# Kernel optimization log

Hardware: AMD Instinct MI355X
Metric: run time of the kernel (lower is better)

The kernel has to match this reference:

```python
import jax, jax.numpy as jnp
import numpy as np

# --- config (Qwen3-Next linear attention defaults) ---
B, S, H = 1, 256, 2048
NK, NV, DK, DV, K = 4, 32, 128, 128, 4
KEY_DIM = NK * DK          # 512
VAL_DIM = NV * DV          # 4096
CONV_DIM = 2 * KEY_DIM + VAL_DIM  # 5120
EPS = 1e-6


def setup_inputs() -> dict:
    key = jax.random.key(0)
    ks = jax.random.split(key, 8)
    rn = lambda k, shape, sc: jax.random.normal(k, shape, jnp.float32) * sc
    return {
        "hidden_states": jax.random.normal(ks[0], (B, S, H), jnp.float32),
        "w_qkvz": rn(ks[1], (2 * KEY_DIM + 2 * VAL_DIM, H), 0.02),  # in_proj_qkvz weight
        "w_ba": rn(ks[2], (2 * NV, H), 0.02),                        # in_proj_ba weight
        "w_out": rn(ks[3], (H, VAL_DIM), 0.02),                      # out_proj weight
        "conv_w": rn(ks[4], (CONV_DIM, 1, K), 0.1),                  # depthwise conv weight [C,1,K]
        "dt_bias": jnp.ones((NV,), jnp.float32),
        "A_log": jnp.zeros((NV,), jnp.float32),
        "norm_w": jnp.ones((DV,), jnp.float32),
    }


def reference(hidden_states, w_qkvz, w_ba, w_out, conv_w, dt_bias, A_log, norm_w):
    b, s, _ = hidden_states.shape
    # input projections (Linear without bias: x @ W.T)
    qkvz = hidden_states @ w_qkvz.T                      # [B,S,9216]
    ba = hidden_states @ w_ba.T                          # [B,S,64]
    q, k, v, z = jnp.split(qkvz, [KEY_DIM, 2 * KEY_DIM, 2 * KEY_DIM + VAL_DIM], axis=-1)
    beta, alpha = jnp.split(ba, 2, axis=-1)              # each [B,S,NV]

    # causal depthwise conv over concat(q,k,v), then silu
    qkv = jnp.concatenate([q, k, v], axis=-1).transpose(0, 2, 1)   # [B,C,S]
    qkv = jax.lax.conv_general_dilated(
        qkv, conv_w, window_strides=(1,), padding=[(K - 1, 0)],
        dimension_numbers=("NCH", "OIH", "NCH"), feature_group_count=CONV_DIM)
    qkv = jax.nn.silu(qkv).transpose(0, 2, 1)            # [B,S,C]
    q, k, v = jnp.split(qkv, [KEY_DIM, 2 * KEY_DIM], axis=-1)

    q = q.reshape(b, s, NK, DK)
    k = k.reshape(b, s, NK, DK)
    v = v.reshape(b, s, NV, DV)
    z = z.reshape(b, s, NV, DV)

    # GQA-style head expansion (repeat_interleave)
    ratio = NV // NK
    q = jnp.repeat(q, ratio, axis=2)                     # [B,S,NV,DK]
    k = jnp.repeat(k, ratio, axis=2)

    # NOTE: original computes g = -softplus(-A_log - alpha) but never uses it (dead code).
    beta_g = jax.nn.sigmoid(beta + dt_bias)[..., None]   # [B,S,NV,1]
    q = q * (DK ** -0.5)

    # naive delta-rule: full outer-product tensor + cumsum (memory-bound)
    kv = jnp.einsum("bsnk,bsnv->bsnkv", k, v * beta_g)   # [B,S,NV,DK,DV]
    out = jnp.einsum("bsnk,bsnkv->bsnv", q, jnp.cumsum(kv, axis=1))  # [B,S,NV,DV]

    # gated RMSNorm over head_v_dim in fp32
    of = out.astype(jnp.float32)
    var = jnp.mean(of * of, axis=-1, keepdims=True)
    of = of * jax.lax.rsqrt(var + EPS) * norm_w
    of = of * jax.nn.silu(z.astype(jnp.float32))

    return of.reshape(b, s, VAL_DIM) @ w_out.T           # [B,S,H]
```

## Files before the change

kernel.cpp:

```cpp
#include <hip/hip_runtime.h>
#include <hip/hip_bf16.h>

#define S_LEN   256
#define HID     2048
#define NVH     32
#define DKD     128
#define DVD     128
#define KEYDIM  512
#define VALDIM  4096
#define CONVDIM 5120
#define QKVZ_N  9216
#define EPS_F   1e-6f

typedef __attribute__((ext_vector_type(8))) short bf16x8;
typedef __attribute__((ext_vector_type(4))) float f32x4;

__device__ __forceinline__ unsigned short f2bf(float f) {
    union { float f; unsigned int i; } v; v.f = f;
    unsigned int x = v.i;
    return (unsigned short)((x + 0x7FFFu + ((x >> 16) & 1u)) >> 16);
}
__device__ __forceinline__ unsigned int pk2(float x, float y) {
    union { __hip_bfloat162 h; unsigned int u; } c;
    c.h = __float22bfloat162_rn(float2{x, y});
    return c.u;
}
__device__ __forceinline__ bf16x8 pack_bf8(float4 lo, float4 hi) {
    union { uint4 u; bf16x8 h; } c;
    c.u.x = pk2(lo.x, lo.y); c.u.y = pk2(lo.z, lo.w);
    c.u.z = pk2(hi.x, hi.y); c.u.w = pk2(hi.z, hi.w);
    return c.h;
}
__device__ __forceinline__ void gl_lds16(const void* g, void* l) {
    __builtin_amdgcn_global_load_lds(
        (const __attribute__((address_space(1))) unsigned int*)g,
        (__attribute__((address_space(3))) unsigned int*)l,
        16, 0, 0);
}

template<int NT>
__global__ __launch_bounds__(256, 2)
void gemm_db(const unsigned short* __restrict__ A, const float* __restrict__ B,
             float* __restrict__ Cpart, int N, int K, int kc) {
    __shared__ __align__(16) unsigned short As[2][128][64];
    __shared__ __align__(16) float Bs[2][NT][64];

    const int tid  = threadIdx.x;
    const int lane = tid & 63, wave = tid >> 6;
    const int wm = wave >> 1, wn = wave & 1;
    const int quad = lane >> 4, l16 = lane & 15;
    const int m0 = blockIdx.y * 128, n0 = blockIdx.x * NT;
    const int kbeg = blockIdx.z * kc;
    const int niter = kc >> 6;

    const int a_ro = lane >> 3;
    const int a_gc = (lane & 7) ^ a_ro;
    const int b_ro = lane >> 4;
    const int b_cs = lane & 15;

    f32x4 acc[4][2];
#pragma unroll
    for (int i = 0; i < 4; i++)
#pragma unroll
        for (int j = 0; j < 2; j++) acc[i][j] = (f32x4){0.f, 0.f, 0.f, 0.f};

    auto stage = [&](int buf, int kk) {
#pragma unroll
        for (int t = 0; t < 4; ++t) {
            int rbase = wave * 32 + t * 8;
            gl_lds16(A + (size_t)(m0 + rbase + a_ro) * K + kk + a_gc * 8,
                     &As[buf][rbase][0]);
        }
#pragma unroll
        for (int t = 0; t < NT / 16; ++t) {
            int rbase = wave * (NT / 4) + t * 4;
            int r = rbase + b_ro;
            int gc = b_cs ^ (r & 7);
            gl_lds16(B + (size_t)(n0 + r) * K + kk + gc * 4,
                     &Bs[buf][rbase][0]);
        }
    };

    auto compute = [&](int buf) {
#pragma unroll
        for (int ks = 0; ks < 2; ++ks) {
            bf16x8 af[4];
#pragma unroll
            for (int i = 0; i < 4; ++i) {
                int r = wm * 64 + i * 16 + l16;
                int c = (ks * 4 + quad) ^ (l16 & 7);
                af[i] = *(const bf16x8*)(&As[buf][r][c * 8]);
            }
#pragma unroll
            for (int j = 0; j < 2; ++j) {
                int r = wn * 32 + j * 16 + l16;
                int x = l16 & 7;
                int c0 = (ks * 8 + quad * 2) ^ x;
                int c1 = (ks * 8 + quad * 2 + 1) ^ x;
                float4 lo = *(const float4*)(&Bs[buf][r][c0 * 4]);
                float4 hi = *(const float4*)(&Bs[buf][r][c1 * 4]);
                bf16x8 bfr = pack_bf8(lo, hi);
#pragma unroll
                for (int i = 0; i < 4; ++i)
                    acc[i][j] = __builtin_amdgcn_mfma_f32_16x16x32_bf16(af[i], bfr, acc[i][j], 0, 0, 0);
            }
        }
    };

    stage(0, kbeg);
    __syncthreads();
    for (int it = 0; it < niter; ++it) {
        if (it + 1 < niter) stage((it + 1) & 1, kbeg + (it + 1) * 64);
        compute(it & 1);
        __syncthreads();
    }

    float* C = Cpart + (size_t)blockIdx.z * 256 * N;
#pragma unroll
    for (int i = 0; i < 4; i++)
#pragma unroll
        for (int j = 0; j < 2; j++)
#pragma unroll
            for (int r = 0; r < 4; r++) {
                int row = m0 + wm * 64 + i * 16 + quad * 4 + r;
                int col = n0 + wn * 32 + j * 16 + l16;
                C[(size_t)row * N + col] = acc[i][j][r];
            }
}

template<int P>
__global__ void reduce_sum(const float* __restrict__ part, float* __restrict__ out, int n) {
    int i = (blockIdx.x * 256 + threadIdx.x) * 4;
    if (i >= n) return;
    float4 s = *(const float4*)(part + i);
#pragma unroll
    for (int p = 1; p < P; p++) {
        float4 v = *(const float4*)(part + (size_t)p * n + i);
        s.x += v.x; s.y += v.y; s.z += v.z; s.w += v.w;
    }
    *(float4*)(out + i) = s;
}

__global__ __launch_bounds__(256)
void ba_proj_cvt(const float* __restrict__ hs, const float* __restrict__ w_ba,
                 float* __restrict__ ba, unsigned short* __restrict__ abf) {
    int s = blockIdx.x;
    int n = threadIdx.x & 63, seg = threadIdx.x >> 6;
    const float* x = hs + (size_t)s * HID + seg * 512;
    const float* w = w_ba + (size_t)n * HID + seg * 512;
    float acc = 0.f;
#pragma unroll 4
    for (int k = 0; k < 512; k += 4) {
        float4 xv = *(const float4*)(x + k);
        float4 wv = *(const float4*)(w + k);
        acc += xv.x * wv.x + xv.y * wv.y + xv.z * wv.z + xv.w * wv.w;
    }
    __shared__ float parts[4][64];
    parts[seg][n] = acc;
    {
        int d = threadIdx.x * 8;
        const float4* p = (const float4*)(hs + (size_t)s * HID + d);
        float4 a = p[0], b = p[1];
        uint4 r;
        r.x = pk2(a.x, a.y); r.y = pk2(a.z, a.w);
        r.z = pk2(b.x, b.y); r.w = pk2(b.z, b.w);
        *(uint4*)(abf + (size_t)s * HID + d) = r;
    }
    __syncthreads();
    if (threadIdx.x < 64)
        ba[s * 64 + threadIdx.x] = parts[0][threadIdx.x] + parts[1][threadIdx.x]
                                 + parts[2][threadIdx.x] + parts[3][threadIdx.x];
}

template<int P>
__global__ __launch_bounds__(256)
void sum_conv(const float* __restrict__ part, const float* __restrict__ conv_w,
              float* __restrict__ conv, float* __restrict__ zs) {
    const int s0 = blockIdx.y * 16;
    const int c  = blockIdx.x * 1024 + threadIdx.x * 4;
    auto sum4 = [&](int s) {
        const float* p = part + (size_t)s * QKVZ_N + c;
        float4 v = *(const float4*)p;
#pragma unroll
        for (int q = 1; q < P; q++) {
            float4 w = *(const float4*)(p + (size_t)q * S_LEN * QKVZ_N);
            v.x += w.x; v.y += w.y; v.z += w.z; v.w += w.w;
        }
        return v;
    };
    if (c < CONVDIM) {
        float4 cw[4];
#pragma unroll
        for (int i = 0; i < 4; ++i) cw[i] = *(const float4*)(conv_w + (size_t)(c + i) * 4);
        float4 w0{0,0,0,0}, w1{0,0,0,0}, w2{0,0,0,0};
        for (int s = (s0 >= 3 ? s0 - 3 : 0); s < s0; ++s) { w0 = w1; w1 = w2; w2 = sum4(s); }
        for (int s = s0; s < s0 + 16; ++s) {
            float4 w3 = sum4(s);
            float4 o;
            o.x = w0.x * cw[0].x + w1.x * cw[0].y + w2.x * cw[0].z + w3.x * cw[0].w;
            o.y = w0.y * cw[1].x + w1.y * cw[1].y + w2.y * cw[1].z + w3.y * cw[1].w;
            o.z = w0.z * cw[2].x + w1.z * cw[2].y + w2.z * cw[2].z + w3.z * cw[2].w;
            o.w = w0.w * cw[3].x + w1.w * cw[3].y + w2.w * cw[3].z + w3.w * cw[3].w;
            o.x = o.x / (1.f + __expf(-o.x));
            o.y = o.y / (1.f + __expf(-o.y));
            o.z = o.z / (1.f + __expf(-o.z));
            o.w = o.w / (1.f + __expf(-o.w));
            *(float4*)(conv + (size_t)s * CONVDIM + c) = o;
            w0 = w1; w1 = w2; w2 = w3;
        }
    } else {
        for (int s = s0; s < s0 + 16; ++s) {
            float4 v = sum4(s);
            *(float4*)(zs + (size_t)s * VALDIM + (c - CONVDIM)) = v;
        }
    }
}

__global__ __launch_bounds__(256)
void scores_k(const float* __restrict__ conv, const float* __restrict__ ba,
              const float* __restrict__ dt_bias, float* __restrict__ scores) {
    if (blockIdx.x > blockIdx.y) return;
    int hk = blockIdx.z;
    int s0 = blockIdx.y * 16, t0 = blockIdx.x * 16;
    __shared__ float Qs[16][132], Ks[16][132];
    int tid = threadIdx.x;
    int qoff = hk * DKD;
    int koff = KEYDIM + hk * DKD;
    for (int idx = tid; idx < 16 * 128; idx += 256) {
        int i = idx >> 7, d = idx & 127;
        Qs[i][d] = conv[(size_t)(s0 + i) * CONVDIM + qoff + d];
        Ks[i][d] = conv[(size_t)(t0 + i) * CONVDIM + koff + d];
    }
    __syncthreads();
    int tx = tid & 15, ty = tid >> 4;
    int s = s0 + ty, t = t0 + tx;
    float dot = 0.f;
    for (int d = 0; d < 128; d++) dot += Qs[ty][d] * Ks[tx][d];
    float base = (t <= s) ? dot * 0.08838834764831845f : 0.f;
#pragma unroll
    for (int v = 0; v < 8; v++) {
        int n = hk * 8 + v;
        float b = ba[t * 64 + n] + dt_bias[n];
        float bg = 1.f / (1.f + __expf(-b));
        scores[((size_t)n * 256 + s) * 256 + t] = base * bg;
    }
}

__global__ __launch_bounds__(256)
void attn_rms(const float* __restrict__ scores, const float* __restrict__ conv,
              const float* __restrict__ zs, const float* __restrict__ norm_w,
              unsigned short* __restrict__ normed) {
    int n = blockIdx.y, s0 = blockIdx.x * 16;
    int voff = 2 * KEYDIM + n * DVD;
    __shared__ float Ss[16][17];
    __shared__ float Vs[16][132];
    int tid = threadIdx.x, sy = tid >> 4, dx = tid & 15;
    float acc[8] = {0.f, 0.f, 0.f, 0.f, 0.f, 0.f, 0.f, 0.f};
    for (int t0 = 0; t0 <= s0; t0 += 16) {
        Ss[sy][dx] = scores[((size_t)n * 256 + s0 + sy) * 256 + t0 + dx];
        const float* vp = conv + (size_t)(t0 + sy) * CONVDIM + voff + dx * 8;
        *(float4*)&Vs[sy][dx * 8]     = *(const float4*)vp;
        *(float4*)&Vs[sy][dx * 8 + 4] = *(const float4*)(vp + 4);
        __syncthreads();
#pragma unroll
        for (int j = 0; j < 16; j++) {
            float sv = Ss[sy][j];
#pragma unroll
            for (int r = 0; r < 8; r++) acc[r] += sv * Vs[j][dx + 16 * r];
        }
        __syncthreads();
    }
    float ssq = 0.f;
#pragma unroll
    for (int r = 0; r < 8; r++) ssq += acc[r] * acc[r];
#pragma unroll
    for (int m = 1; m <= 8; m <<= 1) ssq += __shfl_xor(ssq, m, 64);
    float inv = rsqrtf(ssq * (1.f / 128.f) + EPS_F);
    int s = s0 + sy;
#pragma unroll
    for (int r = 0; r < 8; r++) {
        int d = dx + 16 * r;
        float z = zs[(size_t)s * VALDIM + n * DVD + d];
        float sz = z / (1.f + __expf(-z));
        float v = acc[r] * inv * norm_w[d] * sz;
        normed[((size_t)s * NVH + n) * DVD + d] = f2bf(v);
    }
}

extern "C" void kernel_launch(void* const* d_in, const int* in_sizes, int n_in,
                              void* d_out, int out_size, void* d_ws, size_t ws_size,
                              hipStream_t stream) {
    const float* hs      = (const float*)d_in[0];
    const float* w_qkvz  = (const float*)d_in[1];
    const float* w_ba    = (const float*)d_in[2];
    const float* w_out   = (const float*)d_in[3];
    const float* conv_w  = (const float*)d_in[4];
    const float* dt_bias = (const float*)d_in[5];
    const float* norm_w  = (const float*)d_in[7];

    char* ws = (char*)d_ws;
    unsigned short* abf = (unsigned short*)ws; ws += (size_t)S_LEN * HID * 2;
    float* ba   = (float*)ws;  ws += (size_t)S_LEN * 64 * 4;
    float* conv = (float*)ws;  ws += (size_t)S_LEN * CONVDIM * 4;
    float* zs   = (float*)ws;  ws += (size_t)S_LEN * VALDIM * 4;
    char* regB = ws;
    const bool big = ws_size >= (size_t)50 * 1024 * 1024;
    const int sk1 = big ? 4 : 2;
    const int sk2 = big ? 8 : 4;
    float* scratch1 = (float*)regB;
    unsigned short* normed = (unsigned short*)regB;
    float* scratch2 = (float*)(regB + 2097152);
    float* scores   = (float*)(regB + 2097152 + (size_t)sk2 * 2097152);

    ba_proj_cvt<<<S_LEN, 256, 0, stream>>>(hs, w_ba, ba, abf);
    gemm_db<64><<<dim3(QKVZ_N / 64, 2, sk1), 256, 0, stream>>>(abf, w_qkvz, scratch1, QKVZ_N, HID, HID / sk1);
    if (big) sum_conv<4><<<dim3(9, 16), 256, 0, stream>>>(scratch1, conv_w, conv, zs);
    else     sum_conv<2><<<dim3(9, 16), 256, 0, stream>>>(scratch1, conv_w, conv, zs);
    scores_k<<<dim3(16, 16, 4), 256, 0, stream>>>(conv, ba, dt_bias, scores);
    attn_rms<<<dim3(16, NVH), 256, 0, stream>>>(scores, conv, zs, norm_w, normed);
    gemm_db<64><<<dim3(HID / 64, 2, sk2), 256, 0, stream>>>(normed, w_out, scratch2, HID, VALDIM, VALDIM / sk2);
    if (big) reduce_sum<8><<<(S_LEN * HID) / 1024, 256, 0, stream>>>(scratch2, (float*)d_out, S_LEN * HID);
    else     reduce_sum<4><<<(S_LEN * HID) / 1024, 256, 0, stream>>>(scratch2, (float*)d_out, S_LEN * HID);
}
```

Baseline: 244.7 us.

## Use full-M single-buffer GEMM tiles, deeper split-K, and triangular score grid

The GEMM kernel now covers all 256 rows per block with a single LDS buffer instead of two 128-row double-buffered tiles. Each B tile is then loaded once per block rather than twice, the LDS footprint per block shrinks, and three blocks per CU are requested. The output projection switches to 32-wide N tiles with twice the split-K factor, and sum_conv uses smaller sequence chunks. scores_k now launches only the lower-triangular tile pairs instead of launching the full grid and exiting early. The risks are losing load/compute overlap without double buffering, more partial-sum traffic in the reduction, and a larger workspace requirement for the big path.

Measured after the change: 253.8 us. 1.04x slower.

```diff
diff --git a/kernel.cpp b/kernel.cpp
--- a/kernel.cpp
+++ b/kernel.cpp
@@ -39,37 +39,37 @@
 }
 
 template<int NT>
-__global__ __launch_bounds__(256, 2)
-void gemm_db(const unsigned short* __restrict__ A, const float* __restrict__ B,
+__global__ __launch_bounds__(256, 3)
+void gemm_sn(const unsigned short* __restrict__ A, const float* __restrict__ B,
              float* __restrict__ Cpart, int N, int K, int kc) {
-    __shared__ __align__(16) unsigned short As[2][128][64];
-    __shared__ __align__(16) float Bs[2][NT][64];
+    __shared__ __align__(16) unsigned short As[256][64];
+    __shared__ __align__(16) float Bs[NT][64];
 
     const int tid  = threadIdx.x;
     const int lane = tid & 63, wave = tid >> 6;
-    const int wm = wave >> 1, wn = wave & 1;
     const int quad = lane >> 4, l16 = lane & 15;
-    const int m0 = blockIdx.y * 128, n0 = blockIdx.x * NT;
-    const int kbeg = blockIdx.z * kc;
+    const int n0 = blockIdx.x * NT;
+    const int kbeg = blockIdx.y * kc;
     const int niter = kc >> 6;
+    constexpr int NB = NT / 16;
 
     const int a_ro = lane >> 3;
     const int a_gc = (lane & 7) ^ a_ro;
     const int b_ro = lane >> 4;
     const int b_cs = lane & 15;
 
-    f32x4 acc[4][2];
+    f32x4 acc[4][NB];
 #pragma unroll
     for (int i = 0; i < 4; i++)
 #pragma unroll
-        for (int j = 0; j < 2; j++) acc[i][j] = (f32x4){0.f, 0.f, 0.f, 0.f};
-
-    auto stage = [&](int buf, int kk) {
-#pragma unroll
-        for (int t = 0; t < 4; ++t) {
-            int rbase = wave * 32 + t * 8;
-            gl_lds16(A + (size_t)(m0 + rbase + a_ro) * K + kk + a_gc * 8,
-                     &As[buf][rbase][0]);
+        for (int j = 0; j < NB; j++) acc[i][j] = (f32x4){0.f, 0.f, 0.f, 0.f};
+
+    auto stage = [&](int kk) {
+#pragma unroll
+        for (int t = 0; t < 8; ++t) {
+            int rbase = wave * 64 + t * 8;
+            gl_lds16(A + (size_t)(rbase + a_ro) * K + kk + a_gc * 8,
+                     &As[rbase][0]);
         }
 #pragma unroll
         for (int t = 0; t < NT / 16; ++t) {
@@ -77,28 +77,28 @@
             int r = rbase + b_ro;
             int gc = b_cs ^ (r & 7);
             gl_lds16(B + (size_t)(n0 + r) * K + kk + gc * 4,
-                     &Bs[buf][rbase][0]);
+                     &Bs[rbase][0]);
         }
     };
 
-    auto compute = [&](int buf) {
+    auto compute = [&]() {
 #pragma unroll
         for (int ks = 0; ks < 2; ++ks) {
             bf16x8 af[4];
 #pragma unroll
             for (int i = 0; i < 4; ++i) {
-                int r = wm * 64 + i * 16 + l16;
+                int r = wave * 64 + i * 16 + l16;
                 int c = (ks * 4 + quad) ^ (l16 & 7);
-                af[i] = *(const bf16x8*)(&As[buf][r][c * 8]);
+                af[i] = *(const bf16x8*)(&As[r][c * 8]);
             }
 #pragma unroll
-            for (int j = 0; j < 2; ++j) {
-                int r = wn * 32 + j * 16 + l16;
+            for (int j = 0; j < NB; ++j) {
+                int r = j * 16 + l16;
                 int x = l16 & 7;
                 int c0 = (ks * 8 + quad * 2) ^ x;
                 int c1 = (ks * 8 + quad * 2 + 1) ^ x;
-                float4 lo = *(const float4*)(&Bs[buf][r][c0 * 4]);
-                float4 hi = *(const float4*)(&Bs[buf][r][c1 * 4]);
+                float4 lo = *(const float4*)(&Bs[r][c0 * 4]);
+                float4 hi = *(const float4*)(&Bs[r][c1 * 4]);
                 bf16x8 bfr = pack_bf8(lo, hi);
 #pragma unroll
                 for (int i = 0; i < 4; ++i)
@@ -107,23 +107,25 @@
         }
     };
 
-    stage(0, kbeg);
-    __syncthreads();
+    stage(kbeg);
     for (int it = 0; it < niter; ++it) {
-        if (it + 1 < niter) stage((it + 1) & 1, kbeg + (it + 1) * 64);
-        compute(it & 1);
         __syncthreads();
-    }
-
-    float* C = Cpart + (size_t)blockIdx.z * 256 * N;
+        compute();
+        if (it + 1 < niter) {
+            __syncthreads();
+            stage(kbeg + (it + 1) * 64);
+        }
+    }
+
+    float* C = Cpart + (size_t)blockIdx.y * 256 * N;
 #pragma unroll
     for (int i = 0; i < 4; i++)
 #pragma unroll
-        for (int j = 0; j < 2; j++)
+        for (int j = 0; j < NB; j++)
 #pragma unroll
             for (int r = 0; r < 4; r++) {
-                int row = m0 + wm * 64 + i * 16 + quad * 4 + r;
-                int col = n0 + wn * 32 + j * 16 + l16;
+                int row = wave * 64 + i * 16 + quad * 4 + r;
+                int col = n0 + j * 16 + l16;
                 C[(size_t)row * N + col] = acc[i][j][r];
             }
 }
@@ -176,7 +178,7 @@
 __global__ __launch_bounds__(256)
 void sum_conv(const float* __restrict__ part, const float* __restrict__ conv_w,
               float* __restrict__ conv, float* __restrict__ zs) {
-    const int s0 = blockIdx.y * 16;
+    const int s0 = blockIdx.y * 8;
     const int c  = blockIdx.x * 1024 + threadIdx.x * 4;
     auto sum4 = [&](int s) {
         const float* p = part + (size_t)s * QKVZ_N + c;
@@ -194,7 +196,7 @@
         for (int i = 0; i < 4; ++i) cw[i] = *(const float4*)(conv_w + (size_t)(c + i) * 4);
         float4 w0{0,0,0,0}, w1{0,0,0,0}, w2{0,0,0,0};
         for (int s = (s0 >= 3 ? s0 - 3 : 0); s < s0; ++s) { w0 = w1; w1 = w2; w2 = sum4(s); }
-        for (int s = s0; s < s0 + 16; ++s) {
+        for (int s = s0; s < s0 + 8; ++s) {
             float4 w3 = sum4(s);
             float4 o;
             o.x = w0.x * cw[0].x + w1.x * cw[0].y + w2.x * cw[0].z + w3.x * cw[0].w;
@@ -209,7 +211,7 @@
             w0 = w1; w1 = w2; w2 = w3;
         }
     } else {
-        for (int s = s0; s < s0 + 16; ++s) {
+        for (int s = s0; s < s0 + 8; ++s) {
             float4 v = sum4(s);
             *(float4*)(zs + (size_t)s * VALDIM + (c - CONVDIM)) = v;
         }
@@ -219,9 +221,13 @@
 __global__ __launch_bounds__(256)
 void scores_k(const float* __restrict__ conv, const float* __restrict__ ba,
               const float* __restrict__ dt_bias, float* __restrict__ scores) {
-    if (blockIdx.x > blockIdx.y) return;
-    int hk = blockIdx.z;
-    int s0 = blockIdx.y * 16, t0 = blockIdx.x * 16;
+    int p = blockIdx.x;
+    int st = (int)((__fsqrt_rn(8.f * p + 1.f) - 1.f) * 0.5f);
+    while ((st + 1) * (st + 2) / 2 <= p) st++;
+    while (st * (st + 1) / 2 > p) st--;
+    int tt = p - st * (st + 1) / 2;
+    int hk = blockIdx.y;
+    int s0 = st * 16, t0 = tt * 16;
     __shared__ float Qs[16][132], Ks[16][132];
     int tid = threadIdx.x;
     int qoff = hk * DKD;
@@ -304,21 +310,23 @@
     float* conv = (float*)ws;  ws += (size_t)S_LEN * CONVDIM * 4;
     float* zs   = (float*)ws;  ws += (size_t)S_LEN * VALDIM * 4;
     char* regB = ws;
-    const bool big = ws_size >= (size_t)50 * 1024 * 1024;
+    const bool big = ws_size >= (size_t)56 * 1024 * 1024;
     const int sk1 = big ? 4 : 2;
-    const int sk2 = big ? 8 : 4;
+    const int sk2 = big ? 16 : 8;
     float* scratch1 = (float*)regB;
     unsigned short* normed = (unsigned short*)regB;
     float* scratch2 = (float*)(regB + 2097152);
     float* scores   = (float*)(regB + 2097152 + (size_t)sk2 * 2097152);
 
     ba_proj_cvt<<<S_LEN, 256, 0, stream>>>(hs, w_ba, ba, abf);
-    gemm_db<64><<<dim3(QKVZ_N / 64, 2, sk1), 256, 0, stream>>>(abf, w_qkvz, scratch1, QKVZ_N, HID, HID / sk1);
-    if (big) sum_conv<4><<<dim3(9, 16), 256, 0, stream>>>(scratch1, conv_w, conv, zs);
-    else     sum_conv<2><<<dim3(9, 16), 256, 0, stream>>>(scratch1, conv_w, conv, zs);
-    scores_k<<<dim3(16, 16, 4), 256, 0, stream>>>(conv, ba, dt_bias, scores);
+    if (big) gemm_sn<64><<<dim3(QKVZ_N / 64, 4), 256, 0, stream>>>(abf, w_qkvz, scratch1, QKVZ_N, HID, HID / 4);
+    else     gemm_sn<64><<<dim3(QKVZ_N / 64, 2), 256, 0, stream>>>(abf, w_qkvz, scratch1, QKVZ_N, HID, HID / 2);
+    if (big) sum_conv<4><<<dim3(9, 32), 256, 0, stream>>>(scratch1, conv_w, conv, zs);
+    else     sum_conv<2><<<dim3(9, 32), 256, 0, stream>>>(scratch1, conv_w, conv, zs);
+    scores_k<<<dim3(136, 4), 256, 0, stream>>>(conv, ba, dt_bias, scores);
     attn_rms<<<dim3(16, NVH), 256, 0, stream>>>(scores, conv, zs, norm_w, normed);
-    gemm_db<64><<<dim3(HID / 64, 2, sk2), 256, 0, stream>>>(normed, w_out, scratch2, HID, VALDIM, VALDIM / sk2);
-    if (big) reduce_sum<8><<<(S_LEN * HID) / 1024, 256, 0, stream>>>(scratch2, (float*)d_out, S_LEN * HID);
-    else     reduce_sum<4><<<(S_LEN * HID) / 1024, 256, 0, stream>>>(scratch2, (float*)d_out, S_LEN * HID);
-}
+    if (big) gemm_sn<32><<<dim3(HID / 32, 16), 256, 0, stream>>>(normed, w_out, scratch2, HID, VALDIM, VALDIM / 16);
+    else     gemm_sn<32><<<dim3(HID / 32,  8), 256, 0, stream>>>(normed, w_out, scratch2, HID, VALDIM, VALDIM / 8);
+    if (big) reduce_sum<16><<<(S_LEN * HID) / 1024, 256, 0, stream>>>(scratch2, (float*)d_out, S_LEN * HID);
+    else     reduce_sum<8> <<<(S_LEN * HID) / 1024, 256, 0, stream>>>(scratch2, (float*)d_out, S_LEN * HID);
+}
```
